# Performance work log

Hardware: AMD Instinct MI355X
Metric: run time of the kernel (lower is better)

Reference implementation:

```python
import jax, jax.numpy as jnp
import numpy as np

BN_EPS = 1e-3  # keras BatchNormalization default epsilon


def batch_norm(x):
    # Fresh keras BatchNorm in training mode: gamma=1, beta=0, batch stats over axis 0
    mean = jnp.mean(x, axis=0, keepdims=True)
    var = jnp.var(x, axis=0, keepdims=True)
    return (x - mean) * jax.lax.rsqrt(var + BN_EPS)


def setup_inputs() -> dict:
    key = jax.random.key(0)
    k1, k2, k3 = jax.random.split(key, 3)
    N, D = 100000, 512
    x1 = jax.random.normal(k1, (N, D), dtype=jnp.float32)
    x2 = jax.random.normal(k2, (N, D), dtype=jnp.float32)
    # glorot_uniform for [D, D] kernel
    limit = np.sqrt(6.0 / (D + D)).astype(np.float32)
    kernel = jax.random.uniform(k3, (D, D), dtype=jnp.float32, minval=-limit, maxval=limit)
    return {"x1": x1, "x2": x2, "kernel": kernel}


def reference(x1, x2, kernel):
    b1 = batch_norm(x1)  # [N, D]
    b2 = batch_norm(x2)  # [N, D]
    gate = jax.nn.relu(jnp.tanh(b1 @ kernel))  # [N, D]; dropout_rate=0 -> no dropout
    out = jnp.tanh(b2 * (1.0 - gate) + b1 * gate)
    return out
```

## Files before the change

### kernel.cpp

```cpp
#include <hip/hip_runtime.h>
#include <hip/hip_fp16.h>
#include <stdint.h>

#define N_ROWS 100000
#define DCOLS 512
#define BN_EPS 1e-3f
#define PB 256

typedef __attribute__((ext_vector_type(8))) _Float16 f16x8;
typedef __attribute__((ext_vector_type(4))) float f32x4;
typedef __attribute__((ext_vector_type(4))) unsigned short u16x4;
typedef __attribute__((ext_vector_type(4))) unsigned int u32x4;

__device__ inline float fast_tanh(float x) {
  float e = __expf(2.0f * x);
  return 1.0f - 2.0f * __builtin_amdgcn_rcpf(e + 1.0f);
}
__device__ inline void gld16(const void* g, void* l) {
  __builtin_amdgcn_global_load_lds(
      (const __attribute__((address_space(1))) void*)g,
      (__attribute__((address_space(3))) void*)l, 16, 0, 0);
}
__device__ inline unsigned int h2u(__half2 h) {
  unsigned int u;
  __builtin_memcpy(&u, &h, 4);
  return u;
}
__device__ inline f16x8 u2f(const u32x4& u) {
  f16x8 h;
  __builtin_memcpy(&h, &u, 16);
  return h;
}

__device__ inline void split8h(const float4& v0, const float4& v1,
                               f16x8& hi8, f16x8& lo8) {
  __half2 h0 = __floats2half2_rn(v0.x, v0.y);
  __half2 h1 = __floats2half2_rn(v0.z, v0.w);
  __half2 h2 = __floats2half2_rn(v1.x, v1.y);
  __half2 h3 = __floats2half2_rn(v1.z, v1.w);
  __half2 l0 = __floats2half2_rn(v0.x - __low2float(h0), v0.y - __high2float(h0));
  __half2 l1 = __floats2half2_rn(v0.z - __low2float(h1), v0.w - __high2float(h1));
  __half2 l2 = __floats2half2_rn(v1.x - __low2float(h2), v1.y - __high2float(h2));
  __half2 l3 = __floats2half2_rn(v1.z - __low2float(h3), v1.w - __high2float(h3));
  u32x4 hi = (u32x4){h2u(h0), h2u(h1), h2u(h2), h2u(h3)};
  u32x4 lo = (u32x4){h2u(l0), h2u(l1), h2u(l2), h2u(l3)};
  hi8 = u2f(hi);
  lo8 = u2f(lo);
}

__global__ __launch_bounds__(256) void k_stats_partial(
    const float* __restrict__ x1, const float* __restrict__ x2,
    float* __restrict__ psum, float* __restrict__ psq) {
  const int CH = (N_ROWS + PB - 1) / PB;
  int bx = blockIdx.x;
  int arr = blockIdx.y;
  const float* x = arr ? x2 : x1;
  int r0 = bx * CH;
  int r1 = min(N_ROWS, r0 + CH);
  int c0 = threadIdx.x * 2;
  float s0 = 0.f, s1 = 0.f, q0 = 0.f, q1 = 0.f;
#pragma unroll 8
  for (int r = r0; r < r1; ++r) {
    float2 v = *(const float2*)(x + (size_t)r * DCOLS + c0);
    s0 += v.x; s1 += v.y;
    q0 += v.x * v.x; q1 += v.y * v.y;
  }
  size_t base = ((size_t)(arr * PB + bx)) * DCOLS + c0;
  psum[base] = s0; psum[base + 1] = s1;
  psq[base]  = q0; psq[base + 1]  = q1;
}

__global__ __launch_bounds__(512) void k_stats_final(
    const float* __restrict__ psum, const float* __restrict__ psq,
    float* __restrict__ stats) {
  int a = blockIdx.x;
  int c = threadIdx.x;
  float sa[8], qa[8];
#pragma unroll
  for (int u = 0; u < 8; ++u) { sa[u] = 0.f; qa[u] = 0.f; }
  for (int b = 0; b < PB; b += 8) {
#pragma unroll
    for (int u = 0; u < 8; ++u) {
      size_t base = ((size_t)(a * PB + b + u)) * DCOLS + c;
      sa[u] += psum[base];
      qa[u] += psq[base];
    }
  }
  float s = ((sa[0]+sa[1])+(sa[2]+sa[3]))+((sa[4]+sa[5])+(sa[6]+sa[7]));
  float q = ((qa[0]+qa[1])+(qa[2]+qa[3]))+((qa[4]+qa[5])+(qa[6]+qa[7]));
  float inv = 1.0f / (float)N_ROWS;
  float mean = s * inv;
  float var = q * inv - mean * mean;
  float scale = rsqrtf(var + BN_EPS);
  stats[a * 1024 + c] = scale;
  stats[a * 1024 + 512 + c] = -mean * scale;
}

__global__ __launch_bounds__(256) void k_prepw(
    const float* __restrict__ wk, const float* __restrict__ stats,
    u32x4* __restrict__ wf) {
  int gid = blockIdx.x * 256 + threadIdx.x;
  int j = gid & 511;
  int kg = gid >> 9;
  int k0 = kg * 8;
  unsigned short h[8];
#pragma unroll
  for (int u = 0; u < 8; ++u) {
    float w = wk[(size_t)(k0 + u) * DCOLS + j] * stats[k0 + u];
    __half hh = __float2half_rn(w);
    h[u] = __half_as_ushort(hh);
  }
  int slice = k0 >> 5;
  int lr = (k0 >> 3) & 3;
  int lane = (lr << 4) | (j & 15);
  int g = j >> 4;
  int idx = slice * 2048 + g * 64 + lane;
  u16x4* ph = (u16x4*)&wf[idx];
  u16x4 h0 = {h[0], h[1], h[2], h[3]};
  u16x4 h1 = {h[4], h[5], h[6], h[7]};
  ph[0] = h0; ph[1] = h1;
}

__global__ __launch_bounds__(512) void k_c_partial(
    const float* __restrict__ wk, const float* __restrict__ stats,
    float* __restrict__ cpart) {
  int b = blockIdx.x;
  int j = threadIdx.x;
  const float* negms1 = stats + 512;
  float acc = 0.f;
#pragma unroll
  for (int u = 0; u < 8; ++u) {
    int k = b * 8 + u;
    acc += negms1[k] * wk[(size_t)k * DCOLS + j];
  }
  cpart[b * DCOLS + j] = acc;
}

__global__ __launch_bounds__(512) void k_c_final(
    const float* __restrict__ cpart, float* __restrict__ cvec) {
  int j = threadIdx.x;
  float a = 0.f;
  for (int b = 0; b < 64; ++b) a += cpart[b * DCOLS + j];
  cvec[j] = a;
}

__global__ __launch_bounds__(512, 4) void k_main(
    const float* __restrict__ x1, const float* __restrict__ x2,
    const float* __restrict__ stats, const float* __restrict__ cvec,
    const u32x4* __restrict__ wf, float* __restrict__ out) {
  __shared__ char smem[32768];

  const int tid = threadIdx.x;
  const int lane = tid & 63;
  const int wv = tid >> 6;
  const int ra = lane & 15;
  const int rq = lane >> 4;

  const int xcd = blockIdx.x & 7;
  const int wgid = xcd * 391 + (blockIdx.x >> 3);
  const int panel = wgid >> 2;
  const int q = wgid & 3;
  const int row0 = panel * 128;
  const int col0 = q * 128;

  int arow = row0 + wv * 16 + ra;
  arow = min(arow, N_ROWS - 1);
  const float* abase = x1 + (size_t)arow * DCOLS + rq * 8;

  const u32x4* bsrc[2];
  int bdst[2];
#pragma unroll
  for (int e = 0; e < 2; ++e) {
    int id = wv * 2 + e;
    int kk = id >> 3, g = id & 7;
    bsrc[e] = wf + (size_t)kk * 2048 + (size_t)(q * 8 + g) * 64 + lane;
    bdst[e] = id * 1024;
  }

  f32x4 acc[8];
#pragma unroll
  for (int g = 0; g < 8; ++g) {
    float cj = cvec[col0 + g * 16 + ra];
    acc[g] = (f32x4){cj, cj, cj, cj};
  }

  float4 av[2][4];

  auto stageB = [&](int s, int buf) {
#pragma unroll
    for (int e = 0; e < 2; ++e)
      gld16(bsrc[e] + (size_t)s * 2 * 2048, smem + buf * 16384 + bdst[e]);
  };
  auto loadA = [&](int s, int pset) {
    const float* p = abase + s * 64;
    av[pset][0] = *(const float4*)(p);
    av[pset][1] = *(const float4*)(p + 4);
    av[pset][2] = *(const float4*)(p + 32);
    av[pset][3] = *(const float4*)(p + 36);
  };

  stageB(0, 0);
  asm volatile("" ::: "memory");
  loadA(0, 0);
  asm volatile("s_waitcnt vmcnt(4)" ::: "memory");
  __builtin_amdgcn_s_barrier();
  __builtin_amdgcn_sched_barrier(0);

#pragma unroll
  for (int s = 0; s < 8; ++s) {
    const int p = s & 1;
    if (s < 7) {
      stageB(s + 1, p ^ 1);
      asm volatile("" ::: "memory");
      loadA(s + 1, p ^ 1);
      __builtin_amdgcn_sched_barrier(0);
    }
#pragma unroll
    for (int kk = 0; kk < 2; ++kk) {
      f16x8 bf[8];
#pragma unroll
      for (int g = 0; g < 8; ++g)
        bf[g] = *(const f16x8*)(smem + p * 16384 + (kk * 8 + g) * 1024 +
                                lane * 16);
      f16x8 ah, al;
      split8h(av[p][kk * 2], av[p][kk * 2 + 1], ah, al);
      __builtin_amdgcn_s_setprio(1);
#pragma unroll
      for (int g = 0; g < 8; ++g)
        acc[g] = __builtin_amdgcn_mfma_f32_16x16x32_f16(ah, bf[g], acc[g],
                                                        0, 0, 0);
#pragma unroll
      for (int g = 0; g < 8; ++g)
        acc[g] = __builtin_amdgcn_mfma_f32_16x16x32_f16(al, bf[g], acc[g],
                                                        0, 0, 0);
      __builtin_amdgcn_s_setprio(0);
    }
    if (s < 7) {
      asm volatile("s_waitcnt vmcnt(4)" ::: "memory");
      __builtin_amdgcn_s_barrier();
      __builtin_amdgcn_sched_barrier(0);
    }
  }

  const float* scale1 = stats;
  const float* negms1 = stats + 512;
  const float* scale2 = stats + 1024;
  const float* negms2 = stats + 1536;

  float s1j[8], n1j[8], s2j[8], n2j[8];
#pragma unroll
  for (int g = 0; g < 8; ++g) {
    int j = col0 + g * 16 + ra;
    s1j[g] = scale1[j]; n1j[g] = negms1[j];
    s2j[g] = scale2[j]; n2j[g] = negms2[j];
  }
#pragma unroll
  for (int r = 0; r < 4; ++r) {
    int n = row0 + wv * 16 + rq * 4 + r;
    if (n < N_ROWS) {
#pragma unroll
      for (int g = 0; g < 8; ++g) {
        int j = col0 + g * 16 + ra;
        float c = acc[g][r];
        float tt = fast_tanh(c);
        float gt = fmaxf(tt, 0.0f);
        size_t idx = (size_t)n * DCOLS + j;
        float b1v = fmaf(x1[idx], s1j[g], n1j[g]);
        float b2v = fmaf(x2[idx], s2j[g], n2j[g]);
        out[idx] = fast_tanh(b2v + gt * (b1v - b2v));
      }
    }
  }
}

extern "C" void kernel_launch(void* const* d_in, const int* in_sizes, int n_in,
                              void* d_out, int out_size, void* d_ws, size_t ws_size,
                              hipStream_t stream) {
  const float* x1 = (const float*)d_in[0];
  const float* x2 = (const float*)d_in[1];
  const float* wk = (const float*)d_in[2];
  float* out = (float*)d_out;
  char* ws = (char*)d_ws;

  if (ws_size < (size_t)(4u << 20)) return;

  float* psum  = (float*)ws;
  float* psq   = (float*)(ws + (1 << 20));
  float* stats = (float*)(ws + (2 << 20));
  float* cpart = (float*)(ws + (2 << 20) + (16 << 10));
  float* cvec  = (float*)(ws + (2 << 20) + (160 << 10));
  u32x4* wf    = (u32x4*)(ws + (3 << 20));

  k_stats_partial<<<dim3(PB, 2), 256, 0, stream>>>(x1, x2, psum, psq);
  k_stats_final<<<2, 512, 0, stream>>>(psum, psq, stats);
  k_prepw<<<128, 256, 0, stream>>>(wk, stats, wf);
  k_c_partial<<<64, 512, 0, stream>>>(wk, stats, cpart);
  k_c_final<<<1, 512, 0, stream>>>(cpart, cvec);

  const int nblocks = 8 * 391;
  k_main<<<nblocks, 512, 0, stream>>>(x1, x2, stats, cvec, wf, out);
}
```

Measured before the change: 304.6 us.

## Retile main GEMM to 128x64 blocks with swapped MFMA operands for vectorized epilogue

```diff
diff --git a/kernel.cpp b/kernel.cpp
--- a/kernel.cpp
+++ b/kernel.cpp
@@ -144,11 +144,11 @@
   cvec[j] = a;
 }
 
-__global__ __launch_bounds__(512, 4) void k_main(
+__global__ __launch_bounds__(256, 3) void k_main(
     const float* __restrict__ x1, const float* __restrict__ x2,
     const float* __restrict__ stats, const float* __restrict__ cvec,
     const u32x4* __restrict__ wf, float* __restrict__ out) {
-  __shared__ char smem[32768];
+  __shared__ char smem[16384];
 
   const int tid = threadIdx.x;
   const int lane = tid & 63;
@@ -157,52 +157,62 @@
   const int rq = lane >> 4;
 
   const int xcd = blockIdx.x & 7;
-  const int wgid = xcd * 391 + (blockIdx.x >> 3);
-  const int panel = wgid >> 2;
-  const int q = wgid & 3;
+  const int wgid = xcd * 782 + (blockIdx.x >> 3);
+  const int panel = wgid >> 3;
+  const int oc = wgid & 7;
   const int row0 = panel * 128;
-  const int col0 = q * 128;
-
-  int arow = row0 + wv * 16 + ra;
-  arow = min(arow, N_ROWS - 1);
-  const float* abase = x1 + (size_t)arow * DCOLS + rq * 8;
+  const int col0 = oc * 64;
+
+  const float* abase[2];
+#pragma unroll
+  for (int rg = 0; rg < 2; ++rg) {
+    int r = row0 + wv * 32 + rg * 16 + ra;
+    r = min(r, N_ROWS - 1);
+    abase[rg] = x1 + (size_t)r * DCOLS + rq * 8;
+  }
 
   const u32x4* bsrc[2];
   int bdst[2];
 #pragma unroll
   for (int e = 0; e < 2; ++e) {
     int id = wv * 2 + e;
-    int kk = id >> 3, g = id & 7;
-    bsrc[e] = wf + (size_t)kk * 2048 + (size_t)(q * 8 + g) * 64 + lane;
+    int kk = id >> 2, g = id & 3;
+    bsrc[e] = wf + (size_t)kk * 2048 + (size_t)(oc * 4 + g) * 64 + lane;
     bdst[e] = id * 1024;
   }
 
-  f32x4 acc[8];
-#pragma unroll
-  for (int g = 0; g < 8; ++g) {
-    float cj = cvec[col0 + g * 16 + ra];
-    acc[g] = (f32x4){cj, cj, cj, cj};
-  }
-
-  float4 av[2][4];
+  f32x4 acc[2][4];
+#pragma unroll
+  for (int g = 0; g < 4; ++g) {
+    int j = col0 + g * 16 + rq * 4;
+    float4 cj = *(const float4*)(cvec + j);
+#pragma unroll
+    for (int rg = 0; rg < 2; ++rg)
+      acc[rg][g] = (f32x4){cj.x, cj.y, cj.z, cj.w};
+  }
+
+  float4 av[2][8];
 
   auto stageB = [&](int s, int buf) {
 #pragma unroll
     for (int e = 0; e < 2; ++e)
-      gld16(bsrc[e] + (size_t)s * 2 * 2048, smem + buf * 16384 + bdst[e]);
+      gld16(bsrc[e] + (size_t)s * 4096, smem + buf * 8192 + bdst[e]);
   };
   auto loadA = [&](int s, int pset) {
-    const float* p = abase + s * 64;
-    av[pset][0] = *(const float4*)(p);
-    av[pset][1] = *(const float4*)(p + 4);
-    av[pset][2] = *(const float4*)(p + 32);
-    av[pset][3] = *(const float4*)(p + 36);
+#pragma unroll
+    for (int rg = 0; rg < 2; ++rg) {
+      const float* p = abase[rg] + s * 64;
+      av[pset][rg * 4 + 0] = *(const float4*)(p);
+      av[pset][rg * 4 + 1] = *(const float4*)(p + 4);
+      av[pset][rg * 4 + 2] = *(const float4*)(p + 32);
+      av[pset][rg * 4 + 3] = *(const float4*)(p + 36);
+    }
   };
 
   stageB(0, 0);
   asm volatile("" ::: "memory");
   loadA(0, 0);
-  asm volatile("s_waitcnt vmcnt(4)" ::: "memory");
+  asm volatile("s_waitcnt vmcnt(8)" ::: "memory");
   __builtin_amdgcn_s_barrier();
   __builtin_amdgcn_sched_barrier(0);
 
@@ -217,26 +227,35 @@
     }
 #pragma unroll
     for (int kk = 0; kk < 2; ++kk) {
-      f16x8 bf[8];
-#pragma unroll
-      for (int g = 0; g < 8; ++g)
-        bf[g] = *(const f16x8*)(smem + p * 16384 + (kk * 8 + g) * 1024 +
-                                lane * 16);
-      f16x8 ah, al;
-      split8h(av[p][kk * 2], av[p][kk * 2 + 1], ah, al);
+      f16x8 bfr[4];
+#pragma unroll
+      for (int g = 0; g < 4; ++g)
+        bfr[g] = *(const f16x8*)(smem + p * 8192 + (kk * 4 + g) * 1024 +
+                                 lane * 16);
+      f16x8 xh0, xl0, xh1, xl1;
+      split8h(av[p][0 + kk * 2], av[p][1 + kk * 2], xh0, xl0);
+      split8h(av[p][4 + kk * 2], av[p][5 + kk * 2], xh1, xl1);
       __builtin_amdgcn_s_setprio(1);
 #pragma unroll
-      for (int g = 0; g < 8; ++g)
-        acc[g] = __builtin_amdgcn_mfma_f32_16x16x32_f16(ah, bf[g], acc[g],
-                                                        0, 0, 0);
-#pragma unroll
-      for (int g = 0; g < 8; ++g)
-        acc[g] = __builtin_amdgcn_mfma_f32_16x16x32_f16(al, bf[g], acc[g],
-                                                        0, 0, 0);
+      for (int g = 0; g < 4; ++g)
+        acc[0][g] = __builtin_amdgcn_mfma_f32_16x16x32_f16(bfr[g], xh0,
+                                                           acc[0][g], 0, 0, 0);
+#pragma unroll
+      for (int g = 0; g < 4; ++g)
+        acc[1][g] = __builtin_amdgcn_mfma_f32_16x16x32_f16(bfr[g], xh1,
+                                                           acc[1][g], 0, 0, 0);
+#pragma unroll
+      for (int g = 0; g < 4; ++g)
+        acc[0][g] = __builtin_amdgcn_mfma_f32_16x16x32_f16(bfr[g], xl0,
+                                                           acc[0][g], 0, 0, 0);
+#pragma unroll
+      for (int g = 0; g < 4; ++g)
+        acc[1][g] = __builtin_amdgcn_mfma_f32_16x16x32_f16(bfr[g], xl1,
+                                                           acc[1][g], 0, 0, 0);
       __builtin_amdgcn_s_setprio(0);
     }
     if (s < 7) {
-      asm volatile("s_waitcnt vmcnt(4)" ::: "memory");
+      asm volatile("s_waitcnt vmcnt(8)" ::: "memory");
       __builtin_amdgcn_s_barrier();
       __builtin_amdgcn_sched_barrier(0);
     }
@@ -247,27 +266,46 @@
   const float* scale2 = stats + 1024;
   const float* negms2 = stats + 1536;
 
-  float s1j[8], n1j[8], s2j[8], n2j[8];
-#pragma unroll
-  for (int g = 0; g < 8; ++g) {
-    int j = col0 + g * 16 + ra;
-    s1j[g] = scale1[j]; n1j[g] = negms1[j];
-    s2j[g] = scale2[j]; n2j[g] = negms2[j];
-  }
-#pragma unroll
-  for (int r = 0; r < 4; ++r) {
-    int n = row0 + wv * 16 + rq * 4 + r;
-    if (n < N_ROWS) {
-#pragma unroll
-      for (int g = 0; g < 8; ++g) {
-        int j = col0 + g * 16 + ra;
-        float c = acc[g][r];
-        float tt = fast_tanh(c);
-        float gt = fmaxf(tt, 0.0f);
+#pragma unroll
+  for (int g = 0; g < 4; ++g) {
+    int j = col0 + g * 16 + rq * 4;
+    float4 s1 = *(const float4*)(scale1 + j);
+    float4 n1 = *(const float4*)(negms1 + j);
+    float4 s2 = *(const float4*)(scale2 + j);
+    float4 n2 = *(const float4*)(negms2 + j);
+#pragma unroll
+    for (int rg = 0; rg < 2; ++rg) {
+      int n = row0 + wv * 32 + rg * 16 + ra;
+      if (n < N_ROWS) {
         size_t idx = (size_t)n * DCOLS + j;
-        float b1v = fmaf(x1[idx], s1j[g], n1j[g]);
-        float b2v = fmaf(x2[idx], s2j[g], n2j[g]);
-        out[idx] = fast_tanh(b2v + gt * (b1v - b2v));
+        float4 a1 = *(const float4*)(x1 + idx);
+        float4 a2 = *(const float4*)(x2 + idx);
+        float4 o;
+        {
+          float gt = fmaxf(fast_tanh(acc[rg][g][0]), 0.f);
+          float b1v = fmaf(a1.x, s1.x, n1.x);
+          float b2v = fmaf(a2.x, s2.x, n2.x);
+          o.x = fast_tanh(b2v + gt * (b1v - b2v));
+        }
+        {
+          float gt = fmaxf(fast_tanh(acc[rg][g][1]), 0.f);
+          float b1v = fmaf(a1.y, s1.y, n1.y);
+          float b2v = fmaf(a2.y, s2.y, n2.y);
+          o.y = fast_tanh(b2v + gt * (b1v - b2v));
+        }
+        {
+          float gt = fmaxf(fast_tanh(acc[rg][g][2]), 0.f);
+          float b1v = fmaf(a1.z, s1.z, n1.z);
+          float b2v = fmaf(a2.z, s2.z, n2.z);
+          o.z = fast_tanh(b2v + gt * (b1v - b2v));
+        }
+        {
+          float gt = fmaxf(fast_tanh(acc[rg][g][3]), 0.f);
+          float b1v = fmaf(a1.w, s1.w, n1.w);
+          float b2v = fmaf(a2.w, s2.w, n2.w);
+          o.w = fast_tanh(b2v + gt * (b1v - b2v));
+        }
+        *(float4*)(out + idx) = o;
       }
     }
   }
@@ -297,6 +335,6 @@
   k_c_partial<<<64, 512, 0, stream>>>(wk, stats, cpart);
   k_c_final<<<1, 512, 0, stream>>>(cpart, cvec);
 
-  const int nblocks = 8 * 391;
-  k_main<<<nblocks, 512, 0, stream>>>(x1, x2, stats, cvec, wf, out);
-}
+  const int nblocks = 8 * 782;
+  k_main<<<nblocks, 256, 0, stream>>>(x1, x2, stats, cvec, wf, out);
+}
```

Measured after the change: 395.5 us. 1.3x slower.

## Halve output tile width and preload full weight slice into LDS once

Applied to the files above, without the earlier changes.

```diff
diff --git a/kernel.cpp b/kernel.cpp
--- a/kernel.cpp
+++ b/kernel.cpp
@@ -148,7 +148,7 @@
     const float* __restrict__ x1, const float* __restrict__ x2,
     const float* __restrict__ stats, const float* __restrict__ cvec,
     const u32x4* __restrict__ wf, float* __restrict__ out) {
-  __shared__ char smem[32768];
+  __shared__ char smem[65536];
 
   const int tid = threadIdx.x;
   const int lane = tid & 63;
@@ -157,40 +157,34 @@
   const int rq = lane >> 4;
 
   const int xcd = blockIdx.x & 7;
-  const int wgid = xcd * 391 + (blockIdx.x >> 3);
-  const int panel = wgid >> 2;
-  const int q = wgid & 3;
+  const int wgid = xcd * 782 + (blockIdx.x >> 3);
+  const int panel = wgid >> 3;
+  const int oc = wgid & 7;
   const int row0 = panel * 128;
-  const int col0 = q * 128;
+  const int col0 = oc * 64;
 
   int arow = row0 + wv * 16 + ra;
   arow = min(arow, N_ROWS - 1);
   const float* abase = x1 + (size_t)arow * DCOLS + rq * 8;
 
-  const u32x4* bsrc[2];
-  int bdst[2];
-#pragma unroll
-  for (int e = 0; e < 2; ++e) {
-    int id = wv * 2 + e;
-    int kk = id >> 3, g = id & 7;
-    bsrc[e] = wf + (size_t)kk * 2048 + (size_t)(q * 8 + g) * 64 + lane;
-    bdst[e] = id * 1024;
-  }
-
-  f32x4 acc[8];
-#pragma unroll
-  for (int g = 0; g < 8; ++g) {
-    float cj = cvec[col0 + g * 16 + ra];
-    acc[g] = (f32x4){cj, cj, cj, cj};
+#pragma unroll
+  for (int u = 0; u < 8; ++u) {
+    int id = u * 8 + wv;
+    int slice = id >> 2, cg = id & 3;
+    const u32x4* src =
+        wf + (size_t)slice * 2048 + (size_t)(oc * 4 + cg) * 64 + lane;
+    gld16(src, smem + id * 1024);
+  }
+
+  f32x4 acc[4];
+#pragma unroll
+  for (int cg = 0; cg < 4; ++cg) {
+    float cj = cvec[col0 + cg * 16 + ra];
+    acc[cg] = (f32x4){cj, cj, cj, cj};
   }
 
   float4 av[2][4];
 
-  auto stageB = [&](int s, int buf) {
-#pragma unroll
-    for (int e = 0; e < 2; ++e)
-      gld16(bsrc[e] + (size_t)s * 2 * 2048, smem + buf * 16384 + bdst[e]);
-  };
   auto loadA = [&](int s, int pset) {
     const float* p = abase + s * 64;
     av[pset][0] = *(const float4*)(p);
@@ -199,46 +193,34 @@
     av[pset][3] = *(const float4*)(p + 36);
   };
 
-  stageB(0, 0);
-  asm volatile("" ::: "memory");
   loadA(0, 0);
-  asm volatile("s_waitcnt vmcnt(4)" ::: "memory");
+  asm volatile("s_waitcnt vmcnt(0)" ::: "memory");
   __builtin_amdgcn_s_barrier();
   __builtin_amdgcn_sched_barrier(0);
 
 #pragma unroll
   for (int s = 0; s < 8; ++s) {
     const int p = s & 1;
-    if (s < 7) {
-      stageB(s + 1, p ^ 1);
-      asm volatile("" ::: "memory");
-      loadA(s + 1, p ^ 1);
-      __builtin_amdgcn_sched_barrier(0);
-    }
+    if (s < 7) loadA(s + 1, p ^ 1);
 #pragma unroll
     for (int kk = 0; kk < 2; ++kk) {
-      f16x8 bf[8];
-#pragma unroll
-      for (int g = 0; g < 8; ++g)
-        bf[g] = *(const f16x8*)(smem + p * 16384 + (kk * 8 + g) * 1024 +
-                                lane * 16);
+      f16x8 bfr[4];
+#pragma unroll
+      for (int cg = 0; cg < 4; ++cg)
+        bfr[cg] = *(const f16x8*)(smem + ((s * 2 + kk) * 4 + cg) * 1024 +
+                                  lane * 16);
       f16x8 ah, al;
       split8h(av[p][kk * 2], av[p][kk * 2 + 1], ah, al);
       __builtin_amdgcn_s_setprio(1);
 #pragma unroll
-      for (int g = 0; g < 8; ++g)
-        acc[g] = __builtin_amdgcn_mfma_f32_16x16x32_f16(ah, bf[g], acc[g],
-                                                        0, 0, 0);
-#pragma unroll
-      for (int g = 0; g < 8; ++g)
-        acc[g] = __builtin_amdgcn_mfma_f32_16x16x32_f16(al, bf[g], acc[g],
-                                                        0, 0, 0);
+      for (int cg = 0; cg < 4; ++cg)
+        acc[cg] = __builtin_amdgcn_mfma_f32_16x16x32_f16(ah, bfr[cg], acc[cg],
+                                                         0, 0, 0);
+#pragma unroll
+      for (int cg = 0; cg < 4; ++cg)
+        acc[cg] = __builtin_amdgcn_mfma_f32_16x16x32_f16(al, bfr[cg], acc[cg],
+                                                         0, 0, 0);
       __builtin_amdgcn_s_setprio(0);
-    }
-    if (s < 7) {
-      asm volatile("s_waitcnt vmcnt(4)" ::: "memory");
-      __builtin_amdgcn_s_barrier();
-      __builtin_amdgcn_sched_barrier(0);
     }
   }
 
@@ -247,26 +229,26 @@
   const float* scale2 = stats + 1024;
   const float* negms2 = stats + 1536;
 
-  float s1j[8], n1j[8], s2j[8], n2j[8];
-#pragma unroll
-  for (int g = 0; g < 8; ++g) {
-    int j = col0 + g * 16 + ra;
-    s1j[g] = scale1[j]; n1j[g] = negms1[j];
-    s2j[g] = scale2[j]; n2j[g] = negms2[j];
+  float s1j[4], n1j[4], s2j[4], n2j[4];
+#pragma unroll
+  for (int cg = 0; cg < 4; ++cg) {
+    int j = col0 + cg * 16 + ra;
+    s1j[cg] = scale1[j]; n1j[cg] = negms1[j];
+    s2j[cg] = scale2[j]; n2j[cg] = negms2[j];
   }
 #pragma unroll
   for (int r = 0; r < 4; ++r) {
     int n = row0 + wv * 16 + rq * 4 + r;
     if (n < N_ROWS) {
 #pragma unroll
-      for (int g = 0; g < 8; ++g) {
-        int j = col0 + g * 16 + ra;
-        float c = acc[g][r];
+      for (int cg = 0; cg < 4; ++cg) {
+        int j = col0 + cg * 16 + ra;
+        float c = acc[cg][r];
         float tt = fast_tanh(c);
         float gt = fmaxf(tt, 0.0f);
         size_t idx = (size_t)n * DCOLS + j;
-        float b1v = fmaf(x1[idx], s1j[g], n1j[g]);
-        float b2v = fmaf(x2[idx], s2j[g], n2j[g]);
+        float b1v = fmaf(x1[idx], s1j[cg], n1j[cg]);
+        float b2v = fmaf(x2[idx], s2j[cg], n2j[cg]);
         out[idx] = fast_tanh(b2v + gt * (b1v - b2v));
       }
     }
@@ -297,6 +279,6 @@
   k_c_partial<<<64, 512, 0, stream>>>(wk, stats, cpart);
   k_c_final<<<1, 512, 0, stream>>>(cpart, cvec);
 
-  const int nblocks = 8 * 391;
+  const int nblocks = 8 * 782;
   k_main<<<nblocks, 512, 0, stream>>>(x1, x2, stats, cvec, wf, out);
 }
```

Result: slower. 360.4 us (+18.3%).
